# Kernel tuning notes

Hardware: AMD Instinct MI355X
Metric: run time of the kernel (lower is better)

The kernel has to match this reference:

```python
import jax, jax.numpy as jnp
import numpy as np

BN_EPS = 1e-5


def gcn_conv(x, src, dst, W, b, n_nodes):
    # PyG GCNConv with normalize=True, add_self_loops=True.
    loops = jnp.arange(n_nodes, dtype=src.dtype)
    src_a = jnp.concatenate([src, loops])
    dst_a = jnp.concatenate([dst, loops])
    ones = jnp.ones(src_a.shape[0], dtype=x.dtype)
    deg = jax.ops.segment_sum(ones, dst_a, num_segments=n_nodes)  # [N]
    dinv = jnp.where(deg > 0, jax.lax.rsqrt(deg), 0.0)
    norm = dinv[src_a] * dinv[dst_a]                               # [E+N]
    h = x @ W                                                      # [N, out]
    msg = h[src_a] * norm[:, None]                                 # [E+N, out]
    out = jax.ops.segment_sum(msg, dst_a, num_segments=n_nodes)    # [N, out]
    return out + b


def batch_norm(x, gamma, beta):
    mean = jnp.mean(x, axis=0)
    var = jnp.mean(jnp.square(x - mean), axis=0)  # biased, as in BN training fwd
    return gamma * (x - mean) * jax.lax.rsqrt(var + BN_EPS) + beta


def setup_inputs() -> dict:
    key = jax.random.key(0)
    ks = jax.random.split(key, 8)
    N, E, IN, HID, OUT = 50000, 800000, 128, 64, 40
    node_feat = jax.random.normal(ks[0], (N, IN), dtype=jnp.float32)
    edge_index = jax.random.randint(ks[1], (2, E), 0, N, dtype=jnp.int32)
    s1 = 1.0 / np.sqrt(IN)
    s2 = 1.0 / np.sqrt(HID)
    W1 = jax.random.uniform(ks[2], (IN, HID), jnp.float32, -s1, s1)
    b1 = jax.random.uniform(ks[3], (HID,), jnp.float32, -s1, s1)
    gamma = jnp.ones((HID,), jnp.float32)
    beta = jnp.zeros((HID,), jnp.float32)
    W2 = jax.random.uniform(ks[4], (HID, OUT), jnp.float32, -s2, s2)
    b2 = jax.random.uniform(ks[5], (OUT,), jnp.float32, -s2, s2)
    return {"node_feat": node_feat, "edge_index": edge_index,
            "W1": W1, "b1": b1, "gamma": gamma, "beta": beta,
            "W2": W2, "b2": b2}


def reference(node_feat, edge_index, W1, b1, gamma, beta, W2, b2):
    n_nodes = node_feat.shape[0]
    src, dst = edge_index[0], edge_index[1]
    x = gcn_conv(node_feat, src, dst, W1, b1, n_nodes)
    x = batch_norm(x, gamma, beta)
    x = jax.nn.relu(x)
    # dropout: identity (eval-mode / deterministic baseline)
    x = gcn_conv(x, src, dst, W2, b2, n_nodes)
    return x
```

## Files before the change

kernel.cpp:

```cpp
#include <hip/hip_runtime.h>
#include <hip/hip_fp16.h>

#define N_NODES 50000
#define N_EDGES 800000
#define IN_F    128
#define HID_F   64
#define OUT_F   40

#define EPB   4096
#define NBLK  ((N_EDGES + EPB - 1) / EPB)
#define NBK   ((N_NODES + 255) / 256)
#define CAP   6144
#define NREP  32
#define NB_MM ((N_NODES + 63) / 64)
#define NB_G1 ((N_NODES + 127) / 128)
#define NB_AG ((N_NODES + 31) / 32)

typedef _Float16 half8v __attribute__((ext_vector_type(8)));
typedef float    f32x4  __attribute__((ext_vector_type(4)));

union h8cv { uint4 u; __half h[8]; };


__global__ __launch_bounds__(512) void k_pre(const int* __restrict__ ei,
                                             int* __restrict__ blkcnt,
                                             unsigned int* __restrict__ bket,
                                             float* __restrict__ st2,
                                             const float* __restrict__ x,
                                             const float* __restrict__ W1,
                                             __half* __restrict__ h1r) {
    __shared__ uint4 smem4[3328];
    __shared__ int h[256], fill[256];
    __shared__ int wt[4];
    int t = threadIdx.x;

    if (blockIdx.x < NBLK) {
        unsigned int* staged = (unsigned int*)smem4;
        int lane = t & 63, wv = t >> 6;
        if (t < 256) h[t] = 0;
        if (blockIdx.x == 0)
            for (int i = t; i < NREP * 2 * HID_F; i += 512) st2[i] = 0.f;
        __syncthreads();
        int base = blockIdx.x * EPB;
        int nedge = N_EDGES - base; if (nedge > EPB) nedge = EPB;
#pragma unroll
        for (int it = 0; it < EPB / 512; ++it) {
            int e = base + it * 512 + t;
            if (e < N_EDGES) atomicAdd(&h[ei[N_EDGES + e] >> 8], 1);
        }
        __syncthreads();
        int v = (t < 256) ? h[t] : 0;
        int sv = v;
        if (t < 256) {
#pragma unroll
            for (int o = 1; o < 64; o <<= 1) {
                int u = __shfl_up(sv, o);
                if (lane >= o) sv += u;
            }
            if (lane == 63) wt[wv] = sv;
        }
        __syncthreads();
        if (t < 256) {
            int off = 0;
            if (wv > 0) off += wt[0];
            if (wv > 1) off += wt[1];
            if (wv > 2) off += wt[2];
            fill[t] = sv + off - v;
        }
        __syncthreads();
#pragma unroll
        for (int it = 0; it < EPB / 512; ++it) {
            int e = base + it * 512 + t;
            if (e < N_EDGES) {
                int srcv = ei[e], dstv = ei[N_EDGES + e];
                int p = atomicAdd(&fill[dstv >> 8], 1);
                staged[p] = ((unsigned int)dstv << 16) | (unsigned int)srcv;
            }
        }
        __syncthreads();
        for (int i = t; i < nedge; i += 512) bket[base + i] = staged[i];
        if (t < NBK) blkcnt[t * NBLK + blockIdx.x] = h[t];
        return;
    }

    _Float16 (*sA)[IN_F + 8] = (_Float16(*)[IN_F + 8])smem4;
    _Float16 (*sB)[IN_F + 8] = (_Float16(*)[IN_F + 8])((char*)smem4 + 34816);
    int bid = blockIdx.x - NBLK;
    int row0 = bid * 128;
    for (int i = t; i < 128 * 32; i += 512) {
        int r  = i >> 5;
        int c4 = i & 31;
        int gr = row0 + r;
        float4 v = make_float4(0.f, 0.f, 0.f, 0.f);
        if (gr < N_NODES) v = ((const float4*)x)[gr * 32 + c4];
        sA[r][c4 * 4 + 0] = (_Float16)v.x;
        sA[r][c4 * 4 + 1] = (_Float16)v.y;
        sA[r][c4 * 4 + 2] = (_Float16)v.z;
        sA[r][c4 * 4 + 3] = (_Float16)v.w;
    }
    for (int i = t; i < IN_F * HID_F; i += 512) {
        int k = i >> 6, n = i & 63;
        sB[n][k] = (_Float16)W1[i];
    }
    __syncthreads();

    int lane = t & 63, wid = t >> 6;
    int quad = lane >> 4, l15 = lane & 15;
    int m0 = wid * 16;
    half8v af[4];
#pragma unroll
    for (int ks = 0; ks < 4; ++ks)
        af[ks] = *(const half8v*)&sA[m0 + l15][ks * 32 + quad * 8];
    f32x4 acc[4];
#pragma unroll
    for (int nt = 0; nt < 4; ++nt) acc[nt] = (f32x4)(0.f);
#pragma unroll
    for (int nt = 0; nt < 4; ++nt) {
#pragma unroll
        for (int ks = 0; ks < 4; ++ks) {
            half8v bf = *(const half8v*)&sB[nt * 16 + l15][ks * 32 + quad * 8];
            acc[nt] = __builtin_amdgcn_mfma_f32_16x16x32_f16(af[ks], bf, acc[nt], 0, 0, 0);
        }
    }
    int rbase = row0 + m0 + quad * 4;
#pragma unroll
    for (int nt = 0; nt < 4; ++nt) {
        int col = nt * 16 + l15;
#pragma unroll
        for (int r = 0; r < 4; ++r) {
            int gr = rbase + r;
            if (gr < N_NODES)
                h1r[gr * HID_F + col] = __float2half(acc[nt][r]);
        }
    }
}


__global__ __launch_bounds__(512) void k_bucket(const int* __restrict__ blkcnt,
                                                const unsigned int* __restrict__ bket,
                                                int* __restrict__ rowptr,
                                                float* __restrict__ dinv,
                                                unsigned short* __restrict__ ssrc) {
    __shared__ unsigned int keys[CAP];
    __shared__ unsigned short outb[CAP];
    __shared__ int colpre[256], rowcnt[256], boffs[256];
    __shared__ int cnt[256], fillb[256];
    __shared__ int wt[4], wsum[8], sbase, ssize;
    int b = blockIdx.x, t = threadIdx.x;
    int lane = t & 63, wid = t >> 6;

    int cp = 0, rc = 0;
    if (t < NBLK) {
        for (int bp = 0; bp < b; ++bp) cp += blkcnt[bp * NBLK + t];
        rc = blkcnt[b * NBLK + t];
    }
    if (t < 256) { colpre[t] = cp; rowcnt[t] = rc; }
    int red = cp;
#pragma unroll
    for (int o = 32; o > 0; o >>= 1) red += __shfl_down(red, o);
    if (lane == 0) wsum[wid] = red;
    int sv = rc;
    if (t < 256) {
#pragma unroll
        for (int o = 1; o < 64; o <<= 1) {
            int u = __shfl_up(sv, o);
            if (lane >= o) sv += u;
        }
        if (lane == 63) wt[wid] = sv;
    }
    __syncthreads();
    if (t == 0) {
        int s = 0;
#pragma unroll
        for (int r = 0; r < 8; ++r) s += wsum[r];
        sbase = s;
    }
    if (t < 256) {
        int off = 0;
        if (wid > 0) off += wt[0];
        if (wid > 1) off += wt[1];
        if (wid > 2) off += wt[2];
        boffs[t] = sv + off - rc;
        if (t == 255) ssize = sv + off;
    }
    __syncthreads();
    int base = sbase, size = ssize;

    for (int jj = wid; jj < NBLK; jj += 8) {
        int len = rowcnt[jj];
        int gs  = jj * EPB + colpre[jj];
        int d0  = boffs[jj];
        for (int o = lane; o < len; o += 64) keys[d0 + o] = bket[gs + o];
    }
    if (t < 256) cnt[t] = 0;
    __syncthreads();

    for (int i = t; i < size; i += 512) atomicAdd(&cnt[(keys[i] >> 16) & 255], 1);
    __syncthreads();
    int cv = (t < 256) ? cnt[t] : 0;
    int sv2 = cv;
    if (t < 256) {
#pragma unroll
        for (int o = 1; o < 64; o <<= 1) {
            int u = __shfl_up(sv2, o);
            if (lane >= o) sv2 += u;
        }
        if (lane == 63) wt[wid] = sv2;
    }
    __syncthreads();
    if (t < 256) {
        int off = 0;
        if (wid > 0) off += wt[0];
        if (wid > 1) off += wt[1];
        if (wid > 2) off += wt[2];
        int ex = sv2 + off - cv;
        fillb[t] = ex;
        int node = b * 256 + t;
        if (node < N_NODES) {
            rowptr[node] = base + ex;
            dinv[node]   = rsqrtf((float)cv + 1.0f);
        }
    }
    if (b == 0 && t == 0) rowptr[N_NODES] = N_EDGES;
    __syncthreads();

    for (int i = t; i < size; i += 512) {
        unsigned int k = keys[i];
        int p = atomicAdd(&fillb[(k >> 16) & 255], 1);
        outb[p] = (unsigned short)(k & 0xFFFFu);
    }
    __syncthreads();
    for (int i = t; i < size; i += 512) ssrc[base + i] = outb[i];
}


__global__ __launch_bounds__(256, 8) void k_agg1(const int* __restrict__ rowptr,
                                                 const unsigned short* __restrict__ ssrc,
                                                 const float* __restrict__ dinv,
                                                 const __half* __restrict__ h1r,
                                                 const float* __restrict__ b1,
                                                 __half* __restrict__ agg1h,
                                                 float* __restrict__ st2) {
    __shared__ float vs[32][HID_F + 1];
    int t = threadIdx.x;
    int lane = t & 63, wid = t >> 6;
    int g = lane >> 3, i = lane & 7;
    int rloc = wid * 8 + g;
    int d = blockIdx.x * 32 + rloc;
    bool valid = d < N_NODES;
    int base = 0, end = 0;
    if (valid) { base = rowptr[d]; end = rowptr[d + 1]; }
    float acc[8];
#pragma unroll
    for (int c = 0; c < 8; ++c) acc[c] = 0.f;

    for (int cc = base; cc < end; cc += 8) {
        int nrem = end - cc; if (nrem > 8) nrem = 8;
        int e = (i < nrem) ? (int)ssrc[cc + i] : 0;
#pragma unroll
        for (int kb = 0; kb < 8; kb += 4) {
            if (kb < nrem) {
                int sk[4]; uint4 v[4]; float w[4];
#pragma unroll
                for (int k = 0; k < 4; ++k)
                    sk[k] = __shfl(e, (lane & 56) + kb + k);
#pragma unroll
                for (int k = 0; k < 4; ++k) {
                    if (kb + k < nrem) {
                        v[k] = ((const uint4*)(h1r + (size_t)sk[k] * HID_F))[i];
                        w[k] = dinv[sk[k]];
                    } else { v[k] = make_uint4(0, 0, 0, 0); w[k] = 0.f; }
                }
#pragma unroll
                for (int k = 0; k < 4; ++k) {
                    h8cv cv; cv.u = v[k];
#pragma unroll
                    for (int c = 0; c < 8; ++c)
                        acc[c] += w[k] * __half2float(cv.h[c]);
                }
            }
        }
    }

    float val[8];
    if (valid) {
        float di = dinv[d];
        h8cv self; self.u = ((const uint4*)(h1r + (size_t)d * HID_F))[i];
        const float4 b1a = ((const float4*)b1)[i * 2];
        const float4 b1b = ((const float4*)b1)[i * 2 + 1];
        val[0] = (acc[0] + di * __half2float(self.h[0])) * di + b1a.x;
        val[1] = (acc[1] + di * __half2float(self.h[1])) * di + b1a.y;
        val[2] = (acc[2] + di * __half2float(self.h[2])) * di + b1a.z;
        val[3] = (acc[3] + di * __half2float(self.h[3])) * di + b1a.w;
        val[4] = (acc[4] + di * __half2float(self.h[4])) * di + b1b.x;
        val[5] = (acc[5] + di * __half2float(self.h[5])) * di + b1b.y;
        val[6] = (acc[6] + di * __half2float(self.h[6])) * di + b1b.z;
        val[7] = (acc[7] + di * __half2float(self.h[7])) * di + b1b.w;
        h8cv ov;
#pragma unroll
        for (int c = 0; c < 8; ++c) ov.h[c] = __float2half(val[c]);
        ((uint4*)(agg1h + (size_t)d * HID_F))[i] = ov.u;
    } else {
#pragma unroll
        for (int c = 0; c < 8; ++c) val[c] = 0.f;
    }
#pragma unroll
    for (int c = 0; c < 8; ++c) vs[rloc][i * 8 + c] = val[c];
    __syncthreads();
    if (t < HID_F) {
        float sm = 0.f, s2 = 0.f;
#pragma unroll 4
        for (int r = 0; r < 32; ++r) {
            float v2 = vs[r][t];
            sm += v2; s2 += v2 * v2;
        }
        float* strow = st2 + (blockIdx.x & (NREP - 1)) * (2 * HID_F);
        atomicAdd(&strow[t], sm);
        atomicAdd(&strow[HID_F + t], s2);
    }
}


__global__ __launch_bounds__(256) void k_gemm2(const __half* __restrict__ agg1h,
                                               const float* __restrict__ st2,
                                               const float* __restrict__ gamma,
                                               const float* __restrict__ beta,
                                               const float* __restrict__ W2,
                                               const float* __restrict__ dinv,
                                               __half* __restrict__ h2p) {
    __shared__ _Float16 sA[64][HID_F + 8];
    __shared__ _Float16 sB[48][HID_F + 8];
    __shared__ float sScale[HID_F], sShift[HID_F];
    int t = threadIdx.x;
    if (t < HID_F) {
        float sm = 0.f, s2 = 0.f;
#pragma unroll
        for (int r = 0; r < NREP; ++r) {
            sm += st2[r * (2 * HID_F) + t];
            s2 += st2[r * (2 * HID_F) + HID_F + t];
        }
        float mean = sm * (1.0f / N_NODES);
        float var  = s2 * (1.0f / N_NODES) - mean * mean;
        float inv  = rsqrtf(var + 1e-5f);
        float gv   = gamma[t];
        sScale[t]  = gv * inv;
        sShift[t]  = beta[t] - gv * inv * mean;
    }
    for (int i = t; i < 48 * HID_F; i += 256) {
        int k = i / 48, n = i - k * 48;
        sB[n][k] = (n < OUT_F) ? (_Float16)W2[k * OUT_F + n] : (_Float16)0.f;
    }
    __syncthreads();
    int row0 = blockIdx.x * 64;
    for (int i = t; i < 64 * HID_F; i += 256) {
        int r = i >> 6, k = i & 63;
        int gr = row0 + r;
        float v = 0.f;
        if (gr < N_NODES) {
            float a = __half2float(agg1h[gr * HID_F + k]);
            v = fmaxf(a * sScale[k] + sShift[k], 0.f);
        }
        sA[r][k] = (_Float16)v;
    }
    __syncthreads();

    int lane = t & 63, wid = t >> 6;
    int quad = lane >> 4, l15 = lane & 15;
    int m0 = wid * 16;
    half8v af[2];
#pragma unroll
    for (int ks = 0; ks < 2; ++ks)
        af[ks] = *(const half8v*)&sA[m0 + l15][ks * 32 + quad * 8];
    f32x4 acc[3];
#pragma unroll
    for (int nt = 0; nt < 3; ++nt) acc[nt] = (f32x4)(0.f);
#pragma unroll
    for (int nt = 0; nt < 3; ++nt) {
#pragma unroll
        for (int ks = 0; ks < 2; ++ks) {
            half8v bf = *(const half8v*)&sB[nt * 16 + l15][ks * 32 + quad * 8];
            acc[nt] = __builtin_amdgcn_mfma_f32_16x16x32_f16(af[ks], bf, acc[nt], 0, 0, 0);
        }
    }
    float dv[4];
    int rbase = row0 + m0 + quad * 4;
#pragma unroll
    for (int r = 0; r < 4; ++r)
        dv[r] = (rbase + r < N_NODES) ? dinv[rbase + r] : 0.f;
#pragma unroll
    for (int nt = 0; nt < 3; ++nt) {
        int col = nt * 16 + l15;
        if (col < OUT_F) {
#pragma unroll
            for (int r = 0; r < 4; ++r) {
                int gr = rbase + r;
                if (gr < N_NODES)
                    h2p[(size_t)gr * OUT_F + col] = __float2half(acc[nt][r] * dv[r]);
            }
        }
    }
}


__global__ __launch_bounds__(256, 8) void k_agg2(const int* __restrict__ rowptr,
                                                 const unsigned short* __restrict__ ssrc,
                                                 const float* __restrict__ dinv,
                                                 const __half* __restrict__ h2p,
                                                 const float* __restrict__ b2,
                                                 float* __restrict__ out) {
    int t = threadIdx.x;
    int lane = t & 63, wid = t >> 6;
    int g = lane >> 3, i = lane & 7;
    int rloc = wid * 8 + g;
    int d = blockIdx.x * 32 + rloc;
    bool valid = d < N_NODES;
    int base = 0, end = 0;
    if (valid) { base = rowptr[d]; end = rowptr[d + 1]; }
    float acc[8];
#pragma unroll
    for (int c = 0; c < 8; ++c) acc[c] = 0.f;

    for (int cc = base; cc < end; cc += 8) {
        int nrem = end - cc; if (nrem > 8) nrem = 8;
        int e = (i < nrem) ? (int)ssrc[cc + i] : 0;
#pragma unroll
        for (int kb = 0; kb < 8; kb += 4) {
            if (kb < nrem) {
                int sk[4];
#pragma unroll
                for (int k = 0; k < 4; ++k)
                    sk[k] = __shfl(e, (lane & 56) + kb + k);
                if (i < 5) {
                    uint4 v[4];
#pragma unroll
                    for (int k = 0; k < 4; ++k) {
                        if (kb + k < nrem)
                            v[k] = ((const uint4*)(h2p + (size_t)sk[k] * OUT_F))[i];
                        else v[k] = make_uint4(0, 0, 0, 0);
                    }
#pragma unroll
                    for (int k = 0; k < 4; ++k) {
                        h8cv cv; cv.u = v[k];
#pragma unroll
                        for (int c = 0; c < 8; ++c)
                            acc[c] += __half2float(cv.h[c]);
                    }
                }
            }
        }
    }

    if (valid && i < 5) {
        h8cv self; self.u = ((const uint4*)(h2p + (size_t)d * OUT_F))[i];
        float di = dinv[d];
        const float4 b2a = ((const float4*)b2)[i * 2];
        const float4 b2b = ((const float4*)b2)[i * 2 + 1];
        float4 o0, o1;
        o0.x = (acc[0] + __half2float(self.h[0])) * di + b2a.x;
        o0.y = (acc[1] + __half2float(self.h[1])) * di + b2a.y;
        o0.z = (acc[2] + __half2float(self.h[2])) * di + b2a.z;
        o0.w = (acc[3] + __half2float(self.h[3])) * di + b2a.w;
        o1.x = (acc[4] + __half2float(self.h[4])) * di + b2b.x;
        o1.y = (acc[5] + __half2float(self.h[5])) * di + b2b.y;
        o1.z = (acc[6] + __half2float(self.h[6])) * di + b2b.z;
        o1.w = (acc[7] + __half2float(self.h[7])) * di + b2b.w;
        float4* op = (float4*)(out + (size_t)d * OUT_F + i * 8);
        op[0] = o0;
        op[1] = o1;
    }
}


extern "C" void kernel_launch(void* const* d_in, const int* in_sizes, int n_in,
                              void* d_out, int out_size, void* d_ws, size_t ws_size,
                              hipStream_t stream) {
    const float* x     = (const float*)d_in[0];
    const int*   ei    = (const int*)d_in[1];
    const float* W1    = (const float*)d_in[2];
    const float* b1    = (const float*)d_in[3];
    const float* gamma = (const float*)d_in[4];
    const float* beta  = (const float*)d_in[5];
    const float* W2    = (const float*)d_in[6];
    const float* b2    = (const float*)d_in[7];
    float* out = (float*)d_out;

    char* ws = (char*)d_ws;
    int*            blkcnt = (int*)           (ws + 0);
    int*            rowptr = (int*)           (ws + 154624);
    float*          dinv   = (float*)         (ws + 356352);
    float*          st2    = (float*)         (ws + 558080);
    unsigned int*   bket   = (unsigned int*)  (ws + 574464);
    unsigned short* ssrc   = (unsigned short*)(ws + 3785728);
    __half*         h1r    = (__half*)        (ws + 5387264);
    __half*         agg1h  = (__half*)        (ws + 11787264);
    __half*         h2p    = (__half*)        (ws + 18187264);

    k_pre<<<NBLK + NB_G1, 512, 0, stream>>>(ei, blkcnt, bket, st2, x, W1, h1r);
    k_bucket<<<NBK, 512, 0, stream>>>(blkcnt, bket, rowptr, dinv, ssrc);
    k_agg1<<<NB_AG, 256, 0, stream>>>(rowptr, ssrc, dinv, h1r, b1, agg1h, st2);
    k_gemm2<<<NB_MM, 256, 0, stream>>>(agg1h, st2, gamma, beta, W2, dinv, h2p);
    k_agg2<<<NB_AG, 256, 0, stream>>>(rowptr, ssrc, dinv, h2p, b2, out);
}
```

Baseline: 179.5 us.

## Replace two-pass bucket sort CSR build with degree atomics, scan, and atomic scatter

Replaces the block-local bucketing plus per-bucket sort that built the CSR with a simpler pipeline. Global atomics count in-degrees inside the GEMM kernel, a single-block scan computes rowptr and dinv, and a scatter kernel places source indices with global atomics. This removes the large staged bucket buffer and the complex k_bucket kernel. In exchange it adds a memset, a serial single-block scan over 50k nodes, and heavy contended global atomics. Edge order within each row becomes nondeterministic.

```diff
diff --git a/kernel.cpp b/kernel.cpp
--- a/kernel.cpp
+++ b/kernel.cpp
@@ -7,10 +7,6 @@
 #define HID_F   64
 #define OUT_F   40
 
-#define EPB   4096
-#define NBLK  ((N_EDGES + EPB - 1) / EPB)
-#define NBK   ((N_NODES + 255) / 256)
-#define CAP   6144
 #define NREP  32
 #define NB_MM ((N_NODES + 63) / 64)
 #define NB_G1 ((N_NODES + 127) / 128)
@@ -23,70 +19,18 @@
 
 
 __global__ __launch_bounds__(512) void k_pre(const int* __restrict__ ei,
-                                             int* __restrict__ blkcnt,
-                                             unsigned int* __restrict__ bket,
-                                             float* __restrict__ st2,
                                              const float* __restrict__ x,
                                              const float* __restrict__ W1,
-                                             __half* __restrict__ h1r) {
-    __shared__ uint4 smem4[3328];
-    __shared__ int h[256], fill[256];
-    __shared__ int wt[4];
-    int t = threadIdx.x;
-
-    if (blockIdx.x < NBLK) {
-        unsigned int* staged = (unsigned int*)smem4;
-        int lane = t & 63, wv = t >> 6;
-        if (t < 256) h[t] = 0;
-        if (blockIdx.x == 0)
-            for (int i = t; i < NREP * 2 * HID_F; i += 512) st2[i] = 0.f;
-        __syncthreads();
-        int base = blockIdx.x * EPB;
-        int nedge = N_EDGES - base; if (nedge > EPB) nedge = EPB;
-#pragma unroll
-        for (int it = 0; it < EPB / 512; ++it) {
-            int e = base + it * 512 + t;
-            if (e < N_EDGES) atomicAdd(&h[ei[N_EDGES + e] >> 8], 1);
-        }
-        __syncthreads();
-        int v = (t < 256) ? h[t] : 0;
-        int sv = v;
-        if (t < 256) {
-#pragma unroll
-            for (int o = 1; o < 64; o <<= 1) {
-                int u = __shfl_up(sv, o);
-                if (lane >= o) sv += u;
-            }
-            if (lane == 63) wt[wv] = sv;
-        }
-        __syncthreads();
-        if (t < 256) {
-            int off = 0;
-            if (wv > 0) off += wt[0];
-            if (wv > 1) off += wt[1];
-            if (wv > 2) off += wt[2];
-            fill[t] = sv + off - v;
-        }
-        __syncthreads();
-#pragma unroll
-        for (int it = 0; it < EPB / 512; ++it) {
-            int e = base + it * 512 + t;
-            if (e < N_EDGES) {
-                int srcv = ei[e], dstv = ei[N_EDGES + e];
-                int p = atomicAdd(&fill[dstv >> 8], 1);
-                staged[p] = ((unsigned int)dstv << 16) | (unsigned int)srcv;
-            }
-        }
-        __syncthreads();
-        for (int i = t; i < nedge; i += 512) bket[base + i] = staged[i];
-        if (t < NBK) blkcnt[t * NBLK + blockIdx.x] = h[t];
-        return;
-    }
-
-    _Float16 (*sA)[IN_F + 8] = (_Float16(*)[IN_F + 8])smem4;
-    _Float16 (*sB)[IN_F + 8] = (_Float16(*)[IN_F + 8])((char*)smem4 + 34816);
-    int bid = blockIdx.x - NBLK;
-    int row0 = bid * 128;
+                                             __half* __restrict__ h1r,
+                                             int* __restrict__ deg) {
+    __shared__ _Float16 sA[128][IN_F + 8];
+    __shared__ _Float16 sB[HID_F][IN_F + 8];
+    int t = threadIdx.x;
+
+    for (int e = blockIdx.x * 512 + t; e < N_EDGES; e += NB_G1 * 512)
+        atomicAdd(&deg[ei[N_EDGES + e]], 1);
+
+    int row0 = blockIdx.x * 128;
     for (int i = t; i < 128 * 32; i += 512) {
         int r  = i >> 5;
         int c4 = i & 31;
@@ -136,101 +80,48 @@
 }
 
 
-__global__ __launch_bounds__(512) void k_bucket(const int* __restrict__ blkcnt,
-                                                const unsigned int* __restrict__ bket,
-                                                int* __restrict__ rowptr,
-                                                float* __restrict__ dinv,
-                                                unsigned short* __restrict__ ssrc) {
-    __shared__ unsigned int keys[CAP];
-    __shared__ unsigned short outb[CAP];
-    __shared__ int colpre[256], rowcnt[256], boffs[256];
-    __shared__ int cnt[256], fillb[256];
-    __shared__ int wt[4], wsum[8], sbase, ssize;
-    int b = blockIdx.x, t = threadIdx.x;
-    int lane = t & 63, wid = t >> 6;
-
-    int cp = 0, rc = 0;
-    if (t < NBLK) {
-        for (int bp = 0; bp < b; ++bp) cp += blkcnt[bp * NBLK + t];
-        rc = blkcnt[b * NBLK + t];
-    }
-    if (t < 256) { colpre[t] = cp; rowcnt[t] = rc; }
-    int red = cp;
-#pragma unroll
-    for (int o = 32; o > 0; o >>= 1) red += __shfl_down(red, o);
-    if (lane == 0) wsum[wid] = red;
-    int sv = rc;
-    if (t < 256) {
-#pragma unroll
-        for (int o = 1; o < 64; o <<= 1) {
-            int u = __shfl_up(sv, o);
-            if (lane >= o) sv += u;
-        }
-        if (lane == 63) wt[wid] = sv;
-    }
-    __syncthreads();
-    if (t == 0) {
-        int s = 0;
-#pragma unroll
-        for (int r = 0; r < 8; ++r) s += wsum[r];
-        sbase = s;
-    }
-    if (t < 256) {
-        int off = 0;
-        if (wid > 0) off += wt[0];
-        if (wid > 1) off += wt[1];
-        if (wid > 2) off += wt[2];
-        boffs[t] = sv + off - rc;
-        if (t == 255) ssize = sv + off;
-    }
-    __syncthreads();
-    int base = sbase, size = ssize;
-
-    for (int jj = wid; jj < NBLK; jj += 8) {
-        int len = rowcnt[jj];
-        int gs  = jj * EPB + colpre[jj];
-        int d0  = boffs[jj];
-        for (int o = lane; o < len; o += 64) keys[d0 + o] = bket[gs + o];
-    }
-    if (t < 256) cnt[t] = 0;
-    __syncthreads();
-
-    for (int i = t; i < size; i += 512) atomicAdd(&cnt[(keys[i] >> 16) & 255], 1);
-    __syncthreads();
-    int cv = (t < 256) ? cnt[t] : 0;
-    int sv2 = cv;
-    if (t < 256) {
-#pragma unroll
-        for (int o = 1; o < 64; o <<= 1) {
-            int u = __shfl_up(sv2, o);
-            if (lane >= o) sv2 += u;
-        }
-        if (lane == 63) wt[wid] = sv2;
-    }
-    __syncthreads();
-    if (t < 256) {
-        int off = 0;
-        if (wid > 0) off += wt[0];
-        if (wid > 1) off += wt[1];
-        if (wid > 2) off += wt[2];
-        int ex = sv2 + off - cv;
-        fillb[t] = ex;
-        int node = b * 256 + t;
-        if (node < N_NODES) {
-            rowptr[node] = base + ex;
-            dinv[node]   = rsqrtf((float)cv + 1.0f);
-        }
-    }
-    if (b == 0 && t == 0) rowptr[N_NODES] = N_EDGES;
-    __syncthreads();
-
-    for (int i = t; i < size; i += 512) {
-        unsigned int k = keys[i];
-        int p = atomicAdd(&fillb[(k >> 16) & 255], 1);
-        outb[p] = (unsigned short)(k & 0xFFFFu);
-    }
-    __syncthreads();
-    for (int i = t; i < size; i += 512) ssrc[base + i] = outb[i];
+__global__ __launch_bounds__(1024) void k_scan(const int* __restrict__ deg,
+                                               int* __restrict__ rowptr,
+                                               int* __restrict__ fill,
+                                               float* __restrict__ dinv) {
+    __shared__ int wq[16];
+    int t = threadIdx.x;
+    int lane = t & 63, wv = t >> 6;
+    const int CH = (N_NODES + 1023) / 1024;
+    int s0 = t * CH;
+    int s1 = s0 + CH; if (s1 > N_NODES) s1 = N_NODES;
+    int sum = 0;
+    for (int i = s0; i < s1; ++i) sum += deg[i];
+    int sv = sum;
+#pragma unroll
+    for (int o = 1; o < 64; o <<= 1) {
+        int u = __shfl_up(sv, o);
+        if (lane >= o) sv += u;
+    }
+    if (lane == 63) wq[wv] = sv;
+    __syncthreads();
+    int off = 0;
+    for (int r = 0; r < wv; ++r) off += wq[r];
+    int run = sv + off - sum;
+    for (int i = s0; i < s1; ++i) {
+        int dv = deg[i];
+        rowptr[i] = run;
+        fill[i]   = run;
+        dinv[i]   = rsqrtf((float)dv + 1.0f);
+        run += dv;
+    }
+    if (t == 0) rowptr[N_NODES] = N_EDGES;
+}
+
+
+__global__ __launch_bounds__(512) void k_scatter(const int* __restrict__ ei,
+                                                 int* __restrict__ fill,
+                                                 unsigned short* __restrict__ ssrc) {
+    for (int e = blockIdx.x * 512 + threadIdx.x; e < N_EDGES; e += NB_G1 * 512) {
+        int src = ei[e], dst = ei[N_EDGES + e];
+        int p = atomicAdd(&fill[dst], 1);
+        ssrc[p] = (unsigned short)src;
+    }
 }
 
 
@@ -485,18 +376,20 @@
     float* out = (float*)d_out;
 
     char* ws = (char*)d_ws;
-    int*            blkcnt = (int*)           (ws + 0);
-    int*            rowptr = (int*)           (ws + 154624);
-    float*          dinv   = (float*)         (ws + 356352);
-    float*          st2    = (float*)         (ws + 558080);
-    unsigned int*   bket   = (unsigned int*)  (ws + 574464);
-    unsigned short* ssrc   = (unsigned short*)(ws + 3785728);
-    __half*         h1r    = (__half*)        (ws + 5387264);
-    __half*         agg1h  = (__half*)        (ws + 11787264);
-    __half*         h2p    = (__half*)        (ws + 18187264);
-
-    k_pre<<<NBLK + NB_G1, 512, 0, stream>>>(ei, blkcnt, bket, st2, x, W1, h1r);
-    k_bucket<<<NBK, 512, 0, stream>>>(blkcnt, bket, rowptr, dinv, ssrc);
+    int*            deg    = (int*)           (ws + 0);
+    float*          st2    = (float*)         (ws + 200064);
+    int*            rowptr = (int*)           (ws + 216448);
+    int*            fill   = (int*)           (ws + 416512);
+    float*          dinv   = (float*)         (ws + 616512);
+    unsigned short* ssrc   = (unsigned short*)(ws + 816512);
+    __half*         h1r    = (__half*)        (ws + 2416512);
+    __half*         agg1h  = (__half*)        (ws + 8816512);
+    __half*         h2p    = (__half*)        (ws + 15216512);
+
+    hipMemsetAsync(ws, 0, 216448, stream);
+    k_pre<<<NB_G1, 512, 0, stream>>>(ei, x, W1, h1r, deg);
+    k_scan<<<1, 1024, 0, stream>>>(deg, rowptr, fill, dinv);
+    k_scatter<<<NB_G1, 512, 0, stream>>>(ei, fill, ssrc);
     k_agg1<<<NB_AG, 256, 0, stream>>>(rowptr, ssrc, dinv, h1r, b1, agg1h, st2);
     k_gemm2<<<NB_MM, 256, 0, stream>>>(agg1h, st2, gamma, beta, W2, dinv, h2p);
     k_agg2<<<NB_AG, 256, 0, stream>>>(rowptr, ssrc, dinv, h2p, b2, out);
```

After: 338.8 us. 1.89x slower.

## Split hidden features into two half-width planes and prescale by source dinv

Applied to the files above, without the earlier changes.

The first-layer projection is stored as two 32-column fp16 planes, and k_agg1 aggregates each plane in its own pass. The goal is a smaller gather working set per pass so it fits better in cache. The source-side normalisation is folded into the projected features inside k_bucket, which removes the per-edge dinv gather from the aggregation loop. In exchange, the edge list is walked twice, there is an extra read-modify-write of h1 in k_bucket, and rounding to fp16 a second time after prescaling adds some error.

```diff
diff --git a/kernel.cpp b/kernel.cpp
--- a/kernel.cpp
+++ b/kernel.cpp
@@ -20,6 +20,7 @@
 typedef float    f32x4  __attribute__((ext_vector_type(4)));
 
 union h8cv { uint4 u; __half h[8]; };
+union h4cv { uint2 u; __half h[4]; };
 
 
 __global__ __launch_bounds__(512) void k_pre(const int* __restrict__ ei,
@@ -28,7 +29,8 @@
                                              float* __restrict__ st2,
                                              const float* __restrict__ x,
                                              const float* __restrict__ W1,
-                                             __half* __restrict__ h1r) {
+                                             __half* __restrict__ h1a,
+                                             __half* __restrict__ h1b) {
     __shared__ uint4 smem4[3328];
     __shared__ int h[256], fill[256];
     __shared__ int wt[4];
@@ -126,11 +128,13 @@
 #pragma unroll
     for (int nt = 0; nt < 4; ++nt) {
         int col = nt * 16 + l15;
+        __half* dst = (col < 32) ? h1a : h1b;
+        int c32 = col & 31;
 #pragma unroll
         for (int r = 0; r < 4; ++r) {
             int gr = rbase + r;
             if (gr < N_NODES)
-                h1r[gr * HID_F + col] = __float2half(acc[nt][r]);
+                dst[(size_t)gr * 32 + c32] = __float2half(acc[nt][r]);
         }
     }
 }
@@ -140,11 +144,14 @@
                                                 const unsigned int* __restrict__ bket,
                                                 int* __restrict__ rowptr,
                                                 float* __restrict__ dinv,
-                                                unsigned short* __restrict__ ssrc) {
+                                                unsigned short* __restrict__ ssrc,
+                                                __half* __restrict__ h1a,
+                                                __half* __restrict__ h1b) {
     __shared__ unsigned int keys[CAP];
     __shared__ unsigned short outb[CAP];
     __shared__ int colpre[256], rowcnt[256], boffs[256];
     __shared__ int cnt[256], fillb[256];
+    __shared__ float sdinv[256];
     __shared__ int wt[4], wsum[8], sbase, ssize;
     int b = blockIdx.x, t = threadIdx.x;
     int lane = t & 63, wid = t >> 6;
@@ -217,8 +224,10 @@
         fillb[t] = ex;
         int node = b * 256 + t;
         if (node < N_NODES) {
+            float d = rsqrtf((float)cv + 1.0f);
             rowptr[node] = base + ex;
-            dinv[node]   = rsqrtf((float)cv + 1.0f);
+            dinv[node]   = d;
+            sdinv[t]     = d;
         }
     }
     if (b == 0 && t == 0) rowptr[N_NODES] = N_EDGES;
@@ -231,17 +240,34 @@
     }
     __syncthreads();
     for (int i = t; i < size; i += 512) ssrc[base + i] = outb[i];
+
+    for (int idx = t; idx < 256 * 8; idx += 512) {
+        int r = idx >> 3, q = idx & 7;
+        int node2 = b * 256 + r;
+        if (node2 < N_NODES) {
+            __half* tp = (q < 4) ? (h1a + (size_t)node2 * 32)
+                                 : (h1b + (size_t)node2 * 32);
+            uint4* p4 = (uint4*)tp + (q & 3);
+            h8cv u; u.u = *p4;
+            float dsc = sdinv[r];
+#pragma unroll
+            for (int c = 0; c < 8; ++c)
+                u.h[c] = __float2half(__half2float(u.h[c]) * dsc);
+            *p4 = u.u;
+        }
+    }
 }
 
 
 __global__ __launch_bounds__(256, 8) void k_agg1(const int* __restrict__ rowptr,
                                                  const unsigned short* __restrict__ ssrc,
                                                  const float* __restrict__ dinv,
-                                                 const __half* __restrict__ h1r,
+                                                 const __half* __restrict__ h1a,
+                                                 const __half* __restrict__ h1b,
                                                  const float* __restrict__ b1,
                                                  __half* __restrict__ agg1h,
                                                  float* __restrict__ st2) {
-    __shared__ float vs[32][HID_F + 1];
+    __shared__ float vs[32][33];
     int t = threadIdx.x;
     int lane = t & 63, wid = t >> 6;
     int g = lane >> 3, i = lane & 7;
@@ -250,73 +276,71 @@
     bool valid = d < N_NODES;
     int base = 0, end = 0;
     if (valid) { base = rowptr[d]; end = rowptr[d + 1]; }
-    float acc[8];
-#pragma unroll
-    for (int c = 0; c < 8; ++c) acc[c] = 0.f;
-
-    for (int cc = base; cc < end; cc += 8) {
-        int nrem = end - cc; if (nrem > 8) nrem = 8;
-        int e = (i < nrem) ? (int)ssrc[cc + i] : 0;
-#pragma unroll
-        for (int kb = 0; kb < 8; kb += 4) {
-            if (kb < nrem) {
-                int sk[4]; uint4 v[4]; float w[4];
-#pragma unroll
-                for (int k = 0; k < 4; ++k)
-                    sk[k] = __shfl(e, (lane & 56) + kb + k);
-#pragma unroll
-                for (int k = 0; k < 4; ++k) {
-                    if (kb + k < nrem) {
-                        v[k] = ((const uint4*)(h1r + (size_t)sk[k] * HID_F))[i];
-                        w[k] = dinv[sk[k]];
-                    } else { v[k] = make_uint4(0, 0, 0, 0); w[k] = 0.f; }
-                }
-#pragma unroll
-                for (int k = 0; k < 4; ++k) {
-                    h8cv cv; cv.u = v[k];
-#pragma unroll
-                    for (int c = 0; c < 8; ++c)
-                        acc[c] += w[k] * __half2float(cv.h[c]);
+    float di = valid ? dinv[d] : 0.f;
+
+#pragma unroll
+    for (int p = 0; p < 2; ++p) {
+        const __half* tp = p ? h1b : h1a;
+        float acc[4];
+#pragma unroll
+        for (int c = 0; c < 4; ++c) acc[c] = 0.f;
+
+        for (int cc = base; cc < end; cc += 8) {
+            int nrem = end - cc; if (nrem > 8) nrem = 8;
+            int e = (i < nrem) ? (int)ssrc[cc + i] : 0;
+#pragma unroll
+            for (int kb = 0; kb < 8; kb += 4) {
+                if (kb < nrem) {
+                    int sk[4]; uint2 v[4];
+#pragma unroll
+                    for (int k = 0; k < 4; ++k)
+                        sk[k] = __shfl(e, (lane & 56) + kb + k);
+#pragma unroll
+                    for (int k = 0; k < 4; ++k) {
+                        if (kb + k < nrem)
+                            v[k] = ((const uint2*)(tp + (size_t)sk[k] * 32))[i];
+                        else v[k] = make_uint2(0, 0);
+                    }
+#pragma unroll
+                    for (int k = 0; k < 4; ++k) {
+                        h4cv cv; cv.u = v[k];
+#pragma unroll
+                        for (int c = 0; c < 4; ++c)
+                            acc[c] += __half2float(cv.h[c]);
+                    }
                 }
             }
         }
-    }
-
-    float val[8];
-    if (valid) {
-        float di = dinv[d];
-        h8cv self; self.u = ((const uint4*)(h1r + (size_t)d * HID_F))[i];
-        const float4 b1a = ((const float4*)b1)[i * 2];
-        const float4 b1b = ((const float4*)b1)[i * 2 + 1];
-        val[0] = (acc[0] + di * __half2float(self.h[0])) * di + b1a.x;
-        val[1] = (acc[1] + di * __half2float(self.h[1])) * di + b1a.y;
-        val[2] = (acc[2] + di * __half2float(self.h[2])) * di + b1a.z;
-        val[3] = (acc[3] + di * __half2float(self.h[3])) * di + b1a.w;
-        val[4] = (acc[4] + di * __half2float(self.h[4])) * di + b1b.x;
-        val[5] = (acc[5] + di * __half2float(self.h[5])) * di + b1b.y;
-        val[6] = (acc[6] + di * __half2float(self.h[6])) * di + b1b.z;
-        val[7] = (acc[7] + di * __half2float(self.h[7])) * di + b1b.w;
-        h8cv ov;
-#pragma unroll
-        for (int c = 0; c < 8; ++c) ov.h[c] = __float2half(val[c]);
-        ((uint4*)(agg1h + (size_t)d * HID_F))[i] = ov.u;
-    } else {
-#pragma unroll
-        for (int c = 0; c < 8; ++c) val[c] = 0.f;
-    }
-#pragma unroll
-    for (int c = 0; c < 8; ++c) vs[rloc][i * 8 + c] = val[c];
-    __syncthreads();
-    if (t < HID_F) {
-        float sm = 0.f, s2 = 0.f;
+
+        float val[4];
+        if (valid) {
+            h4cv sf; sf.u = ((const uint2*)(tp + (size_t)d * 32))[i];
+#pragma unroll
+            for (int c = 0; c < 4; ++c)
+                val[c] = (acc[c] + __half2float(sf.h[c])) * di + b1[p * 32 + i * 4 + c];
+            h4cv ov;
+#pragma unroll
+            for (int c = 0; c < 4; ++c) ov.h[c] = __float2half(val[c]);
+            ((uint2*)(agg1h + (size_t)d * HID_F + p * 32))[i] = ov.u;
+        } else {
+#pragma unroll
+            for (int c = 0; c < 4; ++c) val[c] = 0.f;
+        }
+#pragma unroll
+        for (int c = 0; c < 4; ++c) vs[rloc][i * 4 + c] = val[c];
+        __syncthreads();
+        if (t < 32) {
+            float sm = 0.f, s2 = 0.f;
 #pragma unroll 4
-        for (int r = 0; r < 32; ++r) {
-            float v2 = vs[r][t];
-            sm += v2; s2 += v2 * v2;
-        }
-        float* strow = st2 + (blockIdx.x & (NREP - 1)) * (2 * HID_F);
-        atomicAdd(&strow[t], sm);
-        atomicAdd(&strow[HID_F + t], s2);
+            for (int r = 0; r < 32; ++r) {
+                float v2 = vs[r][t];
+                sm += v2; s2 += v2 * v2;
+            }
+            float* strow = st2 + (blockIdx.x & (NREP - 1)) * (2 * HID_F);
+            atomicAdd(&strow[p * 32 + t], sm);
+            atomicAdd(&strow[HID_F + p * 32 + t], s2);
+        }
+        __syncthreads();
     }
 }
 
@@ -491,13 +515,14 @@
     float*          st2    = (float*)         (ws + 558080);
     unsigned int*   bket   = (unsigned int*)  (ws + 574464);
     unsigned short* ssrc   = (unsigned short*)(ws + 3785728);
-    __half*         h1r    = (__half*)        (ws + 5387264);
+    __half*         h1a    = (__half*)        (ws + 5387264);
+    __half*         h1b    = (__half*)        (ws + 8587264);
     __half*         agg1h  = (__half*)        (ws + 11787264);
     __half*         h2p    = (__half*)        (ws + 18187264);
 
-    k_pre<<<NBLK + NB_G1, 512, 0, stream>>>(ei, blkcnt, bket, st2, x, W1, h1r);
-    k_bucket<<<NBK, 512, 0, stream>>>(blkcnt, bket, rowptr, dinv, ssrc);
-    k_agg1<<<NB_AG, 256, 0, stream>>>(rowptr, ssrc, dinv, h1r, b1, agg1h, st2);
+    k_pre<<<NBLK + NB_G1, 512, 0, stream>>>(ei, blkcnt, bket, st2, x, W1, h1a, h1b);
+    k_bucket<<<NBK, 512, 0, stream>>>(blkcnt, bket, rowptr, dinv, ssrc, h1a, h1b);
+    k_agg1<<<NB_AG, 256, 0, stream>>>(rowptr, ssrc, dinv, h1a, h1b, b1, agg1h, st2);
     k_gemm2<<<NB_MM, 256, 0, stream>>>(agg1h, st2, gamma, beta, W2, dinv, h2p);
     k_agg2<<<NB_AG, 256, 0, stream>>>(rowptr, ssrc, dinv, h2p, b2, out);
 }
```

After: 185.2 us. +3.1%, slower.

## Sort nodes by degree within buckets to balance aggregation warps

Applied to the files above, without the earlier changes.

Within each 256-node bucket, nodes are counting-sorted by in-degree into a permutation array, and both aggregation kernels read their destination node through this permutation. The aim is for nodes with similar degree to share a wavefront's 8-lane groups, which cuts divergence where lanes idle waiting for the longest row. It costs an extra permutation write and read plus scattered output writes. Invalid tail nodes get the top bin and keep their id at or above N_NODES, so they still fail the valid check.

```diff
diff --git a/kernel.cpp b/kernel.cpp
--- a/kernel.cpp
+++ b/kernel.cpp
@@ -140,17 +140,20 @@
                                                 const unsigned int* __restrict__ bket,
                                                 int* __restrict__ rowptr,
                                                 float* __restrict__ dinv,
-                                                unsigned short* __restrict__ ssrc) {
+                                                unsigned short* __restrict__ ssrc,
+                                                int* __restrict__ perm) {
     __shared__ unsigned int keys[CAP];
     __shared__ unsigned short outb[CAP];
     __shared__ int colpre[256], rowcnt[256], boffs[256];
     __shared__ int cnt[256], fillb[256];
     __shared__ int wt[4], wsum[8], sbase, ssize;
+    __shared__ int dbin[64], dfl[64];
     int b = blockIdx.x, t = threadIdx.x;
     int lane = t & 63, wid = t >> 6;
 
     int cp = 0, rc = 0;
     if (t < NBLK) {
+#pragma unroll 4
         for (int bp = 0; bp < b; ++bp) cp += blkcnt[bp * NBLK + t];
         rc = blkcnt[b * NBLK + t];
     }
@@ -231,6 +234,31 @@
     }
     __syncthreads();
     for (int i = t; i < size; i += 512) ssrc[base + i] = outb[i];
+
+    if (t < 64) dbin[t] = 0;
+    __syncthreads();
+    int node2 = b * 256 + t;
+    int dg = 63;
+    if (t < 256) {
+        if (node2 < N_NODES) { dg = cv; if (dg > 62) dg = 62; }
+        atomicAdd(&dbin[dg], 1);
+    }
+    __syncthreads();
+    if (t < 64) {
+        int bv = dbin[t];
+        int s = bv;
+#pragma unroll
+        for (int o = 1; o < 64; o <<= 1) {
+            int u = __shfl_up(s, o);
+            if (lane >= o) s += u;
+        }
+        dfl[t] = s - bv;
+    }
+    __syncthreads();
+    if (t < 256) {
+        int r = atomicAdd(&dfl[dg], 1);
+        perm[b * 256 + r] = node2;
+    }
 }
 
 
@@ -239,6 +267,7 @@
                                                  const float* __restrict__ dinv,
                                                  const __half* __restrict__ h1r,
                                                  const float* __restrict__ b1,
+                                                 const int* __restrict__ perm,
                                                  __half* __restrict__ agg1h,
                                                  float* __restrict__ st2) {
     __shared__ float vs[32][HID_F + 1];
@@ -246,7 +275,7 @@
     int lane = t & 63, wid = t >> 6;
     int g = lane >> 3, i = lane & 7;
     int rloc = wid * 8 + g;
-    int d = blockIdx.x * 32 + rloc;
+    int d = perm[blockIdx.x * 32 + rloc];
     bool valid = d < N_NODES;
     int base = 0, end = 0;
     if (valid) { base = rowptr[d]; end = rowptr[d + 1]; }
@@ -407,12 +436,13 @@
                                                  const float* __restrict__ dinv,
                                                  const __half* __restrict__ h2p,
                                                  const float* __restrict__ b2,
+                                                 const int* __restrict__ perm,
                                                  float* __restrict__ out) {
     int t = threadIdx.x;
     int lane = t & 63, wid = t >> 6;
     int g = lane >> 3, i = lane & 7;
     int rloc = wid * 8 + g;
-    int d = blockIdx.x * 32 + rloc;
+    int d = perm[blockIdx.x * 32 + rloc];
     bool valid = d < N_NODES;
     int base = 0, end = 0;
     if (valid) { base = rowptr[d]; end = rowptr[d + 1]; }
@@ -494,10 +524,11 @@
     __half*         h1r    = (__half*)        (ws + 5387264);
     __half*         agg1h  = (__half*)        (ws + 11787264);
     __half*         h2p    = (__half*)        (ws + 18187264);
+    int*            perm   = (int*)           (ws + 22187264);
 
     k_pre<<<NBLK + NB_G1, 512, 0, stream>>>(ei, blkcnt, bket, st2, x, W1, h1r);
-    k_bucket<<<NBK, 512, 0, stream>>>(blkcnt, bket, rowptr, dinv, ssrc);
-    k_agg1<<<NB_AG, 256, 0, stream>>>(rowptr, ssrc, dinv, h1r, b1, agg1h, st2);
+    k_bucket<<<NBK, 512, 0, stream>>>(blkcnt, bket, rowptr, dinv, ssrc, perm);
+    k_agg1<<<NB_AG, 256, 0, stream>>>(rowptr, ssrc, dinv, h1r, b1, perm, agg1h, st2);
     k_gemm2<<<NB_MM, 256, 0, stream>>>(agg1h, st2, gamma, beta, W2, dinv, h2p);
-    k_agg2<<<NB_AG, 256, 0, stream>>>(rowptr, ssrc, dinv, h2p, b2, out);
+    k_agg2<<<NB_AG, 256, 0, stream>>>(rowptr, ssrc, dinv, h2p, b2, perm, out);
 }
```

New measurement: 168.1 us. 6.4% less time.
